# Kernel tuning notes

Measured on AMD Instinct MI355X. Metric: run time of the kernel, lower is better.

The kernel has to match this reference:

```python
import jax, jax.numpy as jnp
import numpy as np

TQ, TV, TA = 40, 64, 40
B = 2048
D = 1280          # per-stream feature dim; 4*D == 10*EMBED
EMBED = 512
EPS = 1e-5


def setup_inputs() -> dict:
    key = jax.random.key(0)
    ks = jax.random.split(key, 10)
    q  = jax.random.normal(ks[0], (TQ, B, D), jnp.float32)
    vq = jax.random.normal(ks[1], (TV, B, D), jnp.float32)
    a  = jax.random.normal(ks[2], (TA, B, D), jnp.float32)
    va = jax.random.normal(ks[3], (TV, B, D), jnp.float32)
    qlen = jax.random.randint(ks[4], (B,), 1, TQ + 1, dtype=jnp.int32)
    alen = jax.random.randint(ks[5], (B,), 1, TA + 1, dtype=jnp.int32)
    # classifier params (xavier-ish init)
    W1 = jax.random.normal(ks[6], (4 * D, EMBED), jnp.float32) * (2.0 / (4 * D + EMBED)) ** 0.5
    b1 = jnp.zeros((EMBED,), jnp.float32)
    gamma = jnp.ones((EMBED,), jnp.float32)
    beta = jnp.zeros((EMBED,), jnp.float32)
    W2 = jax.random.normal(ks[7], (EMBED, 1), jnp.float32) * (2.0 / (EMBED + 1)) ** 0.5
    b2 = jnp.zeros((1,), jnp.float32)
    return dict(question_embedding_v=q, visual_embedding_qu=vq,
                answer_embedding_v_expand=a, visual_embedding_an_expand=va,
                W1=W1, b1=b1, gamma=gamma, beta=beta, W2=W2, b2=b2,
                question_len=qlen, answers_len=alen)


def _masked_mean(x, lens):
    # x: [T, B, D], lens: [B] -> mean over first lens[j] timesteps per sample -> [B, D]
    T = x.shape[0]
    mask = (jnp.arange(T)[:, None] < lens[None, :]).astype(x.dtype)  # [T, B]
    return jnp.einsum('tbd,tb->bd', x, mask) / lens.astype(x.dtype)[:, None]


def reference(question_embedding_v, visual_embedding_qu,
              answer_embedding_v_expand, visual_embedding_an_expand,
              W1, b1, gamma, beta, W2, b2,
              question_len, answers_len):
    q  = _masked_mean(question_embedding_v, question_len)          # [B, D]
    vq = visual_embedding_qu.mean(axis=0)                          # [B, D]
    a  = _masked_mean(answer_embedding_v_expand, answers_len)      # [B, D]
    va = visual_embedding_an_expand.mean(axis=0)                   # [B, D]
    feat = jnp.concatenate([q, vq, a, va], axis=1)                 # [B, 4D] = [B, 10*EMBED]
    # Dropout is identity in eval/reference; BatchNorm1d uses batch stats (training mode).
    h = jax.nn.elu(feat @ W1 + b1)                                 # [B, EMBED]
    mu = h.mean(axis=0)
    var = h.var(axis=0)                                            # biased, like torch BN
    h = (h - mu) * jax.lax.rsqrt(var + EPS) * gamma + beta
    return h @ W2 + b2                                             # [B, 1]
```

## Files before the change

### kernel.cpp

```cpp
#include <hip/hip_runtime.h>
#include <hip/hip_bf16.h>

typedef __attribute__((ext_vector_type(8))) short bf16x8;
typedef __attribute__((ext_vector_type(4))) float f32x4;

#define NB 2048
#define ND 1280
#define NK 5120
#define NE 512

static __device__ inline unsigned short f2bf(float x) {
    union { float f; unsigned u; } c; c.f = x;
    unsigned r = c.u + 0x7FFFu + ((c.u >> 16) & 1u);
    return (unsigned short)(r >> 16);
}

__global__ __launch_bounds__(256) void reduce_kernel(
    const float4* __restrict__ q, const float4* __restrict__ vq,
    const float4* __restrict__ aa, const float4* __restrict__ va,
    const int* __restrict__ qlen, const int* __restrict__ alen,
    ushort4* __restrict__ feat)
{
    const int tid = blockIdx.x * 256 + threadIdx.x;
    const int per_seg = NB * 160;
    const int seg = tid / per_seg;
    const int r = tid - seg * per_seg;
    const int b = r / 160;
    const int ch = r - b * 160;

    const long base = (long)b * 320 + ch;
    const long stride = (long)NB * 320;

    float4 a0 = make_float4(0.f, 0.f, 0.f, 0.f);
    float4 a1 = make_float4(0.f, 0.f, 0.f, 0.f);
    float inv;

    if (seg == 1 || seg == 3) {
        const float4* src = (seg == 1) ? vq : va;
        #pragma unroll 8
        for (int t = 0; t < 64; ++t) {
            float4 v0 = src[base + (long)t * stride];
            float4 v1 = src[base + 160 + (long)t * stride];
            a0.x += v0.x; a0.y += v0.y; a0.z += v0.z; a0.w += v0.w;
            a1.x += v1.x; a1.y += v1.y; a1.z += v1.z; a1.w += v1.w;
        }
        inv = 1.0f / 64.0f;
    } else {
        const float4* src = (seg == 0) ? q : aa;
        const int len = (seg == 0) ? qlen[b] : alen[b];
        #pragma unroll 4
        for (int t = 0; t < len; ++t) {
            float4 v0 = src[base + (long)t * stride];
            float4 v1 = src[base + 160 + (long)t * stride];
            a0.x += v0.x; a0.y += v0.y; a0.z += v0.z; a0.w += v0.w;
            a1.x += v1.x; a1.y += v1.y; a1.z += v1.z; a1.w += v1.w;
        }
        inv = 1.0f / (float)len;
    }

    ushort4 o0, o1;
    o0.x = f2bf(a0.x * inv); o0.y = f2bf(a0.y * inv);
    o0.z = f2bf(a0.z * inv); o0.w = f2bf(a0.w * inv);
    o1.x = f2bf(a1.x * inv); o1.y = f2bf(a1.y * inv);
    o1.z = f2bf(a1.z * inv); o1.w = f2bf(a1.w * inv);
    const long fb = (long)b * (NK / 4) + seg * 320 + ch;
    feat[fb] = o0;
    feat[fb + 160] = o1;
}

__global__ __launch_bounds__(256) void w1t_kernel(
    const float* __restrict__ W1, unsigned short* __restrict__ w1t,
    float* __restrict__ s1s2)
{
    if (blockIdx.x == 0) {
        ((float4*)s1s2)[threadIdx.x] = make_float4(0.f, 0.f, 0.f, 0.f);
    }
    __shared__ unsigned short lds[32][33];
    const int bid = blockIdx.x;
    const int kb = (bid >> 4) * 32;
    const int nb = (bid & 15) * 32;
    const int tx = threadIdx.x & 31;
    const int ty = threadIdx.x >> 5;
    #pragma unroll
    for (int i = 0; i < 4; ++i) {
        int k = kb + ty + i * 8;
        lds[ty + i * 8][tx] = f2bf(W1[(long)k * NE + nb + tx]);
    }
    __syncthreads();
    #pragma unroll
    for (int i = 0; i < 4; ++i) {
        int n = nb + ty + i * 8;
        w1t[(long)n * NK + kb + tx] = lds[tx][ty + i * 8];
    }
}

__global__ __launch_bounds__(256) void gemm_kernel(
    const unsigned short* __restrict__ feat, const unsigned short* __restrict__ w1t,
    float* __restrict__ hpart)
{
    __shared__ int4 As[64 * 9];
    __shared__ int4 Bs[64 * 9];

    const int bid = blockIdx.x;
    const int tile = bid & 255;
    const int s = bid >> 8;
    const int m0 = (tile >> 3) << 6;
    const int n0 = (tile & 7) << 6;
    const int kbeg = s * (NK / 4);

    const int t = threadIdx.x;
    const int l = t & 63;
    const int w = t >> 6;
    const int wm = (w >> 1) * 32;
    const int wn = (w & 1) * 32;
    const int srow = t >> 3;
    const int scol = t & 7;

    f32x4 acc[2][2] = {};

    for (int k0 = kbeg; k0 < kbeg + NK / 4; k0 += 64) {
        const unsigned short* Ag = feat + (long)(m0 + srow) * NK + k0 + scol * 8;
        const unsigned short* Bg = w1t + (long)(n0 + srow) * NK + k0 + scol * 8;
        int4 a0 = *(const int4*)Ag;
        int4 a1 = *(const int4*)(Ag + 32L * NK);
        int4 b0 = *(const int4*)Bg;
        int4 b1v = *(const int4*)(Bg + 32L * NK);
        As[srow * 9 + scol] = a0;
        As[(srow + 32) * 9 + scol] = a1;
        Bs[srow * 9 + scol] = b0;
        Bs[(srow + 32) * 9 + scol] = b1v;
        __syncthreads();
        #pragma unroll
        for (int kk = 0; kk < 2; ++kk) {
            const int kc = kk * 4 + (l >> 4);
            bf16x8 af0 = *(const bf16x8*)&As[(wm + (l & 15)) * 9 + kc];
            bf16x8 af1 = *(const bf16x8*)&As[(wm + 16 + (l & 15)) * 9 + kc];
            bf16x8 bf0 = *(const bf16x8*)&Bs[(wn + (l & 15)) * 9 + kc];
            bf16x8 bf1 = *(const bf16x8*)&Bs[(wn + 16 + (l & 15)) * 9 + kc];
            acc[0][0] = __builtin_amdgcn_mfma_f32_16x16x32_bf16(af0, bf0, acc[0][0], 0, 0, 0);
            acc[0][1] = __builtin_amdgcn_mfma_f32_16x16x32_bf16(af0, bf1, acc[0][1], 0, 0, 0);
            acc[1][0] = __builtin_amdgcn_mfma_f32_16x16x32_bf16(af1, bf0, acc[1][0], 0, 0, 0);
            acc[1][1] = __builtin_amdgcn_mfma_f32_16x16x32_bf16(af1, bf1, acc[1][1], 0, 0, 0);
        }
        __syncthreads();
    }

    float* hp = hpart + (long)s * NB * NE;
    const int rbase = m0 + wm + ((l >> 4) << 2);
    const int cbase = n0 + wn + (l & 15);
    #pragma unroll
    for (int mi = 0; mi < 2; ++mi)
        #pragma unroll
        for (int ni = 0; ni < 2; ++ni)
            #pragma unroll
            for (int rr = 0; rr < 4; ++rr)
                hp[(long)(rbase + mi * 16 + rr) * NE + cbase + ni * 16] = acc[mi][ni][rr];
}

__global__ __launch_bounds__(256) void combine_kernel(
    const float* __restrict__ hpart, const float* __restrict__ b1,
    float* __restrict__ h, float* __restrict__ s1s2)
{
    const int blk = blockIdx.x;
    const int t = threadIdx.x;
    const int c = t * 2;
    const float bx = b1[c], by = b1[c + 1];
    float s1x = 0.f, s1y = 0.f, s2x = 0.f, s2y = 0.f;
    const float2* hp = (const float2*)hpart;
    float2* h2 = (float2*)h;
    const long SL = (long)NB * NE / 2;
    #pragma unroll
    for (int i = 0; i < 8; ++i) {
        long row = (long)blk * 8 + i;
        long idx = row * (NE / 2) + t;
        float2 v0 = hp[idx];
        float2 v1 = hp[idx + SL];
        float2 v2 = hp[idx + 2 * SL];
        float2 v3 = hp[idx + 3 * SL];
        float hx = v0.x + v1.x + v2.x + v3.x + bx;
        float hy = v0.y + v1.y + v2.y + v3.y + by;
        hx = hx > 0.f ? hx : expm1f(hx);
        hy = hy > 0.f ? hy : expm1f(hy);
        h2[idx] = make_float2(hx, hy);
        s1x += hx; s2x += hx * hx;
        s1y += hy; s2y += hy * hy;
    }
    unsafeAtomicAdd(&s1s2[c], s1x);
    unsafeAtomicAdd(&s1s2[c + 1], s1y);
    unsafeAtomicAdd(&s1s2[NE + c], s2x);
    unsafeAtomicAdd(&s1s2[NE + c + 1], s2y);
}

__global__ __launch_bounds__(256) void out_kernel(
    const float* __restrict__ h, const float* __restrict__ s1s2,
    const float* __restrict__ gamma, const float* __restrict__ beta,
    const float* __restrict__ W2, const float* __restrict__ b2,
    float* __restrict__ out)
{
    __shared__ float coef[NE];
    __shared__ float red[256];
    const int t = threadIdx.x;

    float term = 0.f;
    #pragma unroll
    for (int i = 0; i < 2; ++i) {
        const int e = t + i * 256;
        const float s1 = s1s2[e];
        const float s2 = s1s2[NE + e];
        const float mu = s1 * (1.0f / NB);
        const float var = s2 * (1.0f / NB) - mu * mu;
        const float rs = rsqrtf(var + 1e-5f);
        const float g = gamma[e], wv = W2[e];
        coef[e] = rs * g * wv;
        term += (beta[e] - mu * rs * g) * wv;
    }
    red[t] = term;
    __syncthreads();
    #pragma unroll
    for (int off = 128; off > 0; off >>= 1) {
        if (t < off) red[t] += red[t + off];
        __syncthreads();
    }
    const float cst = red[0] + b2[0];

    const int w = t >> 6;
    const int l = t & 63;
    const int row = blockIdx.x * 4 + w;
    const float4* h4 = (const float4*)(h + (long)row * NE);
    float4 x0 = h4[l * 2], x1 = h4[l * 2 + 1];
    float4 c0 = *(const float4*)&coef[l * 8];
    float4 c1 = *(const float4*)&coef[l * 8 + 4];
    float dot = x0.x * c0.x + x0.y * c0.y + x0.z * c0.z + x0.w * c0.w
              + x1.x * c1.x + x1.y * c1.y + x1.z * c1.z + x1.w * c1.w;
    #pragma unroll
    for (int off = 32; off > 0; off >>= 1) dot += __shfl_down(dot, off);
    if (l == 0) out[row] = dot + cst;
}

extern "C" void kernel_launch(void* const* d_in, const int* in_sizes, int n_in,
                              void* d_out, int out_size, void* d_ws, size_t ws_size,
                              hipStream_t stream)
{
    const float* q    = (const float*)d_in[0];
    const float* vq   = (const float*)d_in[1];
    const float* aa   = (const float*)d_in[2];
    const float* va   = (const float*)d_in[3];
    const float* W1   = (const float*)d_in[4];
    const float* b1   = (const float*)d_in[5];
    const float* gam  = (const float*)d_in[6];
    const float* bet  = (const float*)d_in[7];
    const float* W2   = (const float*)d_in[8];
    const float* b2   = (const float*)d_in[9];
    const int* qlen   = (const int*)d_in[10];
    const int* alen   = (const int*)d_in[11];
    float* out = (float*)d_out;

    char* ws = (char*)d_ws;
    unsigned short* feat = (unsigned short*)ws;
    unsigned short* w1t  = (unsigned short*)(ws + 20971520);
    float* hbuf          = (float*)(ws + 26214400);
    float* hpart         = (float*)(ws + 30408704);
    float* s1s2          = (float*)(ws + 47185920);

    reduce_kernel<<<5120, 256, 0, stream>>>(
        (const float4*)q, (const float4*)vq, (const float4*)aa, (const float4*)va,
        qlen, alen, (ushort4*)feat);

    w1t_kernel<<<2560, 256, 0, stream>>>(W1, w1t, s1s2);

    gemm_kernel<<<1024, 256, 0, stream>>>(feat, w1t, hpart);

    combine_kernel<<<256, 256, 0, stream>>>(hpart, b1, hbuf, s1s2);

    out_kernel<<<512, 256, 0, stream>>>(hbuf, s1s2, gam, bet, W2, b2, out);
}
```

Baseline: 398.0 us.

## Fuse W1 transpose into reduce, drop split-K and fuse bias/ELU/stats into GEMM

Merges the W1 bf16 transpose blocks into the reduction kernel launch as extra blocks, and switches the input stream loads to nontemporal. The GEMM no longer splits K four ways. It uses 32x64 tiles over the full K and fuses bias, ELU, h store and BatchNorm sum/sumsq atomics into its epilogue. This removes the hpart round trip and the combine kernel, but leaves 512 GEMM blocks each running the full K, so there is less parallelism per tile.

Measured after the change: 375.6 us. 1.06x faster.

```diff
diff --git a/kernel.cpp b/kernel.cpp
--- a/kernel.cpp
+++ b/kernel.cpp
@@ -15,12 +15,39 @@
     return (unsigned short)(r >> 16);
 }
 
-__global__ __launch_bounds__(256) void reduce_kernel(
-    const float4* __restrict__ q, const float4* __restrict__ vq,
-    const float4* __restrict__ aa, const float4* __restrict__ va,
+__global__ __launch_bounds__(256) void reduce_w1t_kernel(
+    const f32x4* __restrict__ q, const f32x4* __restrict__ vq,
+    const f32x4* __restrict__ aa, const f32x4* __restrict__ va,
     const int* __restrict__ qlen, const int* __restrict__ alen,
-    ushort4* __restrict__ feat)
-{
+    ushort4* __restrict__ feat,
+    const float* __restrict__ W1, unsigned short* __restrict__ w1t,
+    float* __restrict__ s1s2)
+{
+    __shared__ unsigned short lds[32][33];
+
+    if (blockIdx.x >= 5120) {
+        const int bid = blockIdx.x - 5120;
+        if (bid == 0) {
+            ((f32x4*)s1s2)[threadIdx.x] = (f32x4){0.f, 0.f, 0.f, 0.f};
+        }
+        const int kb = (bid >> 4) * 32;
+        const int nb = (bid & 15) * 32;
+        const int tx = threadIdx.x & 31;
+        const int ty = threadIdx.x >> 5;
+        #pragma unroll
+        for (int i = 0; i < 4; ++i) {
+            int k = kb + ty + i * 8;
+            lds[ty + i * 8][tx] = f2bf(W1[(long)k * NE + nb + tx]);
+        }
+        __syncthreads();
+        #pragma unroll
+        for (int i = 0; i < 4; ++i) {
+            int n = nb + ty + i * 8;
+            w1t[(long)n * NK + kb + tx] = lds[tx][ty + i * 8];
+        }
+        return;
+    }
+
     const int tid = blockIdx.x * 256 + threadIdx.x;
     const int per_seg = NB * 160;
     const int seg = tid / per_seg;
@@ -31,29 +58,29 @@
     const long base = (long)b * 320 + ch;
     const long stride = (long)NB * 320;
 
-    float4 a0 = make_float4(0.f, 0.f, 0.f, 0.f);
-    float4 a1 = make_float4(0.f, 0.f, 0.f, 0.f);
+    f32x4 a0 = {0.f, 0.f, 0.f, 0.f};
+    f32x4 a1 = {0.f, 0.f, 0.f, 0.f};
     float inv;
 
     if (seg == 1 || seg == 3) {
-        const float4* src = (seg == 1) ? vq : va;
+        const f32x4* src = (seg == 1) ? vq : va;
         #pragma unroll 8
         for (int t = 0; t < 64; ++t) {
-            float4 v0 = src[base + (long)t * stride];
-            float4 v1 = src[base + 160 + (long)t * stride];
-            a0.x += v0.x; a0.y += v0.y; a0.z += v0.z; a0.w += v0.w;
-            a1.x += v1.x; a1.y += v1.y; a1.z += v1.z; a1.w += v1.w;
+            f32x4 v0 = __builtin_nontemporal_load(&src[base + (long)t * stride]);
+            f32x4 v1 = __builtin_nontemporal_load(&src[base + 160 + (long)t * stride]);
+            a0 += v0;
+            a1 += v1;
         }
         inv = 1.0f / 64.0f;
     } else {
-        const float4* src = (seg == 0) ? q : aa;
+        const f32x4* src = (seg == 0) ? q : aa;
         const int len = (seg == 0) ? qlen[b] : alen[b];
         #pragma unroll 4
         for (int t = 0; t < len; ++t) {
-            float4 v0 = src[base + (long)t * stride];
-            float4 v1 = src[base + 160 + (long)t * stride];
-            a0.x += v0.x; a0.y += v0.y; a0.z += v0.z; a0.w += v0.w;
-            a1.x += v1.x; a1.y += v1.y; a1.z += v1.z; a1.w += v1.w;
+            f32x4 v0 = __builtin_nontemporal_load(&src[base + (long)t * stride]);
+            f32x4 v1 = __builtin_nontemporal_load(&src[base + 160 + (long)t * stride]);
+            a0 += v0;
+            a1 += v1;
         }
         inv = 1.0f / (float)len;
     }
@@ -68,127 +95,68 @@
     feat[fb + 160] = o1;
 }
 
-__global__ __launch_bounds__(256) void w1t_kernel(
-    const float* __restrict__ W1, unsigned short* __restrict__ w1t,
-    float* __restrict__ s1s2)
-{
-    if (blockIdx.x == 0) {
-        ((float4*)s1s2)[threadIdx.x] = make_float4(0.f, 0.f, 0.f, 0.f);
-    }
-    __shared__ unsigned short lds[32][33];
-    const int bid = blockIdx.x;
-    const int kb = (bid >> 4) * 32;
-    const int nb = (bid & 15) * 32;
-    const int tx = threadIdx.x & 31;
-    const int ty = threadIdx.x >> 5;
-    #pragma unroll
-    for (int i = 0; i < 4; ++i) {
-        int k = kb + ty + i * 8;
-        lds[ty + i * 8][tx] = f2bf(W1[(long)k * NE + nb + tx]);
-    }
-    __syncthreads();
-    #pragma unroll
-    for (int i = 0; i < 4; ++i) {
-        int n = nb + ty + i * 8;
-        w1t[(long)n * NK + kb + tx] = lds[tx][ty + i * 8];
-    }
-}
-
 __global__ __launch_bounds__(256) void gemm_kernel(
     const unsigned short* __restrict__ feat, const unsigned short* __restrict__ w1t,
-    float* __restrict__ hpart)
-{
-    __shared__ int4 As[64 * 9];
+    const float* __restrict__ b1,
+    float* __restrict__ h, float* __restrict__ s1s2)
+{
+    __shared__ int4 As[32 * 9];
     __shared__ int4 Bs[64 * 9];
 
     const int bid = blockIdx.x;
-    const int tile = bid & 255;
-    const int s = bid >> 8;
-    const int m0 = (tile >> 3) << 6;
-    const int n0 = (tile & 7) << 6;
-    const int kbeg = s * (NK / 4);
+    const int m0 = (bid >> 3) << 5;
+    const int n0 = (bid & 7) << 6;
 
     const int t = threadIdx.x;
     const int l = t & 63;
     const int w = t >> 6;
-    const int wm = (w >> 1) * 32;
-    const int wn = (w & 1) * 32;
+    const int wm = (w >> 1) << 4;
+    const int wn = (w & 1) << 5;
     const int srow = t >> 3;
     const int scol = t & 7;
 
-    f32x4 acc[2][2] = {};
-
-    for (int k0 = kbeg; k0 < kbeg + NK / 4; k0 += 64) {
-        const unsigned short* Ag = feat + (long)(m0 + srow) * NK + k0 + scol * 8;
-        const unsigned short* Bg = w1t + (long)(n0 + srow) * NK + k0 + scol * 8;
-        int4 a0 = *(const int4*)Ag;
-        int4 a1 = *(const int4*)(Ag + 32L * NK);
-        int4 b0 = *(const int4*)Bg;
-        int4 b1v = *(const int4*)(Bg + 32L * NK);
-        As[srow * 9 + scol] = a0;
-        As[(srow + 32) * 9 + scol] = a1;
-        Bs[srow * 9 + scol] = b0;
+    f32x4 acc[2] = {};
+
+    for (int k0 = 0; k0 < NK; k0 += 64) {
+        int4 av = *(const int4*)(feat + (long)(m0 + srow) * NK + k0 + scol * 8);
+        int4 b0v = *(const int4*)(w1t + (long)(n0 + srow) * NK + k0 + scol * 8);
+        int4 b1v = *(const int4*)(w1t + (long)(n0 + 32 + srow) * NK + k0 + scol * 8);
+        As[srow * 9 + scol] = av;
+        Bs[srow * 9 + scol] = b0v;
         Bs[(srow + 32) * 9 + scol] = b1v;
         __syncthreads();
         #pragma unroll
         for (int kk = 0; kk < 2; ++kk) {
             const int kc = kk * 4 + (l >> 4);
-            bf16x8 af0 = *(const bf16x8*)&As[(wm + (l & 15)) * 9 + kc];
-            bf16x8 af1 = *(const bf16x8*)&As[(wm + 16 + (l & 15)) * 9 + kc];
+            bf16x8 af = *(const bf16x8*)&As[(wm + (l & 15)) * 9 + kc];
             bf16x8 bf0 = *(const bf16x8*)&Bs[(wn + (l & 15)) * 9 + kc];
             bf16x8 bf1 = *(const bf16x8*)&Bs[(wn + 16 + (l & 15)) * 9 + kc];
-            acc[0][0] = __builtin_amdgcn_mfma_f32_16x16x32_bf16(af0, bf0, acc[0][0], 0, 0, 0);
-            acc[0][1] = __builtin_amdgcn_mfma_f32_16x16x32_bf16(af0, bf1, acc[0][1], 0, 0, 0);
-            acc[1][0] = __builtin_amdgcn_mfma_f32_16x16x32_bf16(af1, bf0, acc[1][0], 0, 0, 0);
-            acc[1][1] = __builtin_amdgcn_mfma_f32_16x16x32_bf16(af1, bf1, acc[1][1], 0, 0, 0);
-        }
-        __syncthreads();
-    }
-
-    float* hp = hpart + (long)s * NB * NE;
+            acc[0] = __builtin_amdgcn_mfma_f32_16x16x32_bf16(af, bf0, acc[0], 0, 0, 0);
+            acc[1] = __builtin_amdgcn_mfma_f32_16x16x32_bf16(af, bf1, acc[1], 0, 0, 0);
+        }
+        __syncthreads();
+    }
+
     const int rbase = m0 + wm + ((l >> 4) << 2);
-    const int cbase = n0 + wn + (l & 15);
-    #pragma unroll
-    for (int mi = 0; mi < 2; ++mi)
-        #pragma unroll
-        for (int ni = 0; ni < 2; ++ni)
-            #pragma unroll
-            for (int rr = 0; rr < 4; ++rr)
-                hp[(long)(rbase + mi * 16 + rr) * NE + cbase + ni * 16] = acc[mi][ni][rr];
-}
-
-__global__ __launch_bounds__(256) void combine_kernel(
-    const float* __restrict__ hpart, const float* __restrict__ b1,
-    float* __restrict__ h, float* __restrict__ s1s2)
-{
-    const int blk = blockIdx.x;
-    const int t = threadIdx.x;
-    const int c = t * 2;
-    const float bx = b1[c], by = b1[c + 1];
-    float s1x = 0.f, s1y = 0.f, s2x = 0.f, s2y = 0.f;
-    const float2* hp = (const float2*)hpart;
-    float2* h2 = (float2*)h;
-    const long SL = (long)NB * NE / 2;
-    #pragma unroll
-    for (int i = 0; i < 8; ++i) {
-        long row = (long)blk * 8 + i;
-        long idx = row * (NE / 2) + t;
-        float2 v0 = hp[idx];
-        float2 v1 = hp[idx + SL];
-        float2 v2 = hp[idx + 2 * SL];
-        float2 v3 = hp[idx + 3 * SL];
-        float hx = v0.x + v1.x + v2.x + v3.x + bx;
-        float hy = v0.y + v1.y + v2.y + v3.y + by;
-        hx = hx > 0.f ? hx : expm1f(hx);
-        hy = hy > 0.f ? hy : expm1f(hy);
-        h2[idx] = make_float2(hx, hy);
-        s1x += hx; s2x += hx * hx;
-        s1y += hy; s2y += hy * hy;
-    }
-    unsafeAtomicAdd(&s1s2[c], s1x);
-    unsafeAtomicAdd(&s1s2[c + 1], s1y);
-    unsafeAtomicAdd(&s1s2[NE + c], s2x);
-    unsafeAtomicAdd(&s1s2[NE + c + 1], s2y);
+    #pragma unroll
+    for (int ni = 0; ni < 2; ++ni) {
+        const int col = n0 + wn + ni * 16 + (l & 15);
+        const float bias = b1[col];
+        float s1 = 0.f, s2 = 0.f;
+        #pragma unroll
+        for (int rr = 0; rr < 4; ++rr) {
+            float v = acc[ni][rr] + bias;
+            v = v > 0.f ? v : expm1f(v);
+            h[(long)(rbase + rr) * NE + col] = v;
+            s1 += v; s2 += v * v;
+        }
+        s1 += __shfl_xor(s1, 16); s2 += __shfl_xor(s2, 16);
+        s1 += __shfl_xor(s1, 32); s2 += __shfl_xor(s2, 32);
+        if (l < 16) {
+            unsafeAtomicAdd(&s1s2[col], s1);
+            unsafeAtomicAdd(&s1s2[NE + col], s2);
+        }
+    }
 }
 
 __global__ __launch_bounds__(256) void out_kernel(
@@ -226,10 +194,10 @@
     const int w = t >> 6;
     const int l = t & 63;
     const int row = blockIdx.x * 4 + w;
-    const float4* h4 = (const float4*)(h + (long)row * NE);
-    float4 x0 = h4[l * 2], x1 = h4[l * 2 + 1];
-    float4 c0 = *(const float4*)&coef[l * 8];
-    float4 c1 = *(const float4*)&coef[l * 8 + 4];
+    const f32x4* h4 = (const f32x4*)(h + (long)row * NE);
+    f32x4 x0 = h4[l * 2], x1 = h4[l * 2 + 1];
+    f32x4 c0 = *(const f32x4*)&coef[l * 8];
+    f32x4 c1 = *(const f32x4*)&coef[l * 8 + 4];
     float dot = x0.x * c0.x + x0.y * c0.y + x0.z * c0.z + x0.w * c0.w
               + x1.x * c1.x + x1.y * c1.y + x1.z * c1.z + x1.w * c1.w;
     #pragma unroll
@@ -259,18 +227,13 @@
     unsigned short* feat = (unsigned short*)ws;
     unsigned short* w1t  = (unsigned short*)(ws + 20971520);
     float* hbuf          = (float*)(ws + 26214400);
-    float* hpart         = (float*)(ws + 30408704);
-    float* s1s2          = (float*)(ws + 47185920);
-
-    reduce_kernel<<<5120, 256, 0, stream>>>(
-        (const float4*)q, (const float4*)vq, (const float4*)aa, (const float4*)va,
-        qlen, alen, (ushort4*)feat);
-
-    w1t_kernel<<<2560, 256, 0, stream>>>(W1, w1t, s1s2);
-
-    gemm_kernel<<<1024, 256, 0, stream>>>(feat, w1t, hpart);
-
-    combine_kernel<<<256, 256, 0, stream>>>(hpart, b1, hbuf, s1s2);
+    float* s1s2          = (float*)(ws + 30408704);
+
+    reduce_w1t_kernel<<<7680, 256, 0, stream>>>(
+        (const f32x4*)q, (const f32x4*)vq, (const f32x4*)aa, (const f32x4*)va,
+        qlen, alen, (ushort4*)feat, W1, w1t, s1s2);
+
+    gemm_kernel<<<512, 256, 0, stream>>>(feat, w1t, b1, hbuf, s1s2);
 
     out_kernel<<<512, 256, 0, stream>>>(hbuf, s1s2, gam, bet, W2, b2, out);
 }
```
